# Kernel tuning notes

Hardware: AMD Instinct MI355X
Metric: run time of the kernel (lower is better)

Reference implementation:

```python
import jax, jax.numpy as jnp
import numpy as np

N_HEADS = 8

def setup_inputs() -> dict:
    key = jax.random.key(0)
    ks = jax.random.split(key, 8)
    N, D, H = 20000, 16, 256
    scale = np.float32(0.02)
    return {
        "h": jax.random.normal(ks[0], (N, H), dtype=jnp.float32),
        "attention_mask": jnp.zeros((N,), dtype=jnp.float32),
        "neighbor_idx": jax.random.randint(ks[1], (N, D), 0, N, dtype=jnp.int32),
        "Wq": jax.random.normal(ks[2], (H, H), dtype=jnp.float32) * scale,
        "bq": jnp.zeros((H,), dtype=jnp.float32),
        "Wk": jax.random.normal(ks[3], (H, H), dtype=jnp.float32) * scale,
        "bk": jnp.zeros((H,), dtype=jnp.float32),
        "Wv": jax.random.normal(ks[4], (H, H), dtype=jnp.float32) * scale,
        "bv": jnp.zeros((H,), dtype=jnp.float32),
    }

def reference(h, attention_mask, neighbor_idx, Wq, bq, Wk, bk, Wv, bv):
    N, H = h.shape
    nh = N_HEADS
    dh = H // nh
    inv_sqrt_dh = np.float32(1.0 / np.sqrt(dh))
    # query from each node's own state: [N, nh, dh]
    q = (h @ Wq.T + bq).reshape(N, nh, dh)
    # gather neighbor mailbox: [N, D, H]
    nb = h[neighbor_idx]
    k = (nb @ Wk.T + bk).reshape(N, -1, nh, dh)  # [N, D, nh, dh]
    v = (nb @ Wv.T + bv).reshape(N, -1, nh, dh)
    # scores: [N, nh, D]
    scores = jnp.einsum('nhd,nkhd->nhk', q, k) * inv_sqrt_dh
    # additive mask gathered from source nodes, broadcast over heads
    scores = scores + attention_mask[neighbor_idx][:, None, :]
    probs = jax.nn.softmax(scores, axis=-1)
    # dropout prob = 0.0 (eval) -> identity
    ctx = jnp.einsum('nhk,nkhd->nhd', probs, v).reshape(N, H)
    return ctx
```

## Files before the change

### kernel.cpp

```cpp
#include <hip/hip_runtime.h>
#include <hip/hip_fp16.h>
#include <math.h>

#define HDIM 256
#define DNEIGH 16

typedef __attribute__((ext_vector_type(8))) short short8;
typedef __attribute__((ext_vector_type(4))) float f32x4;

static __device__ __forceinline__ unsigned short f2bf(float f) {
    unsigned int u = __float_as_uint(f);
    unsigned int r = (u + 0x7fffu + ((u >> 16) & 1u)) >> 16;
    return (unsigned short)r;
}
static __device__ __forceinline__ float bf_lo(unsigned int u) {
    return __uint_as_float(u << 16);
}
static __device__ __forceinline__ float bf_hi(unsigned int u) {
    return __uint_as_float(u & 0xffff0000u);
}

#if __has_builtin(__builtin_amdgcn_cvt_pk_fp8_f32)
static __device__ __forceinline__ unsigned char f2fp8(float v) {
    int pk = __builtin_amdgcn_cvt_pk_fp8_f32(v, v, 0, false);
    return (unsigned char)(pk & 0xff);
}
#else
static __device__ __forceinline__ unsigned char f2fp8(float v) {
    unsigned short h = __half_as_ushort(__float2half(v * (1.0f / 256.0f)));
    unsigned short mag = h & 0x7fffu;
    mag = (unsigned short)((mag + 0x40u) >> 7);
    if (mag > 0x7f) mag = 0x7f;
    return (unsigned char)(((h >> 8) & 0x80u) | mag);
}
#endif

#if __has_builtin(__builtin_amdgcn_cvt_f32_fp8)
#define FP8D(u, i) __builtin_amdgcn_cvt_f32_fp8((u), (i))
#else
static __device__ __forceinline__ float fp8_byte_dec(unsigned int b) {
    unsigned int hb = ((b & 0x80u) << 8) | ((b & 0x7fu) << 7);
    return __half2float(__ushort_as_half((unsigned short)hb)) * 256.0f;
}
#define FP8D(u, i) fp8_byte_dec(((u) >> ((i) * 8)) & 0xffu)
#endif

static __device__ __forceinline__ void async_copy16(const void* g, void* l) {
    __builtin_amdgcn_global_load_lds(
        (const __attribute__((address_space(1))) unsigned int*)g,
        (__attribute__((address_space(3))) unsigned int*)l, 16, 0, 0);
}

__global__ __launch_bounds__(256) void cvt_kernel(
    const float* __restrict__ h,
    const float* __restrict__ wq, const float* __restrict__ wk, const float* __restrict__ wv,
    unsigned short* __restrict__ hb,
    unsigned short* __restrict__ wqb, unsigned short* __restrict__ wkb, unsigned short* __restrict__ wvb,
    int nh4)
{
    int i = blockIdx.x * 256 + threadIdx.x;
    const int total = nh4 + 3 * 16384;
    if (i >= total) return;
    const float4* src; unsigned short* dst; int off;
    if (i < nh4) { src = (const float4*)h; dst = hb; off = i; }
    else {
        int j = i - nh4; int s = j >> 14; off = j & 16383;
        src = (s == 0) ? (const float4*)wq : (s == 1) ? (const float4*)wk : (const float4*)wv;
        dst = (s == 0) ? wqb : (s == 1) ? wkb : wvb;
    }
    float4 v = src[off];
    ushort4 o;
    o.x = f2bf(v.x); o.y = f2bf(v.y); o.z = f2bf(v.z); o.w = f2bf(v.w);
    *(ushort4*)&dst[off * 4] = o;
}

__global__ __launch_bounds__(256) void qkv_mfma_kernel(
    const unsigned short* __restrict__ hb,
    const unsigned short* __restrict__ Wqb,
    const unsigned short* __restrict__ Wkb,
    const unsigned short* __restrict__ Wvb,
    const float* __restrict__ bq, const float* __restrict__ bk, const float* __restrict__ bv,
    unsigned short* __restrict__ Qb, unsigned char* __restrict__ K8,
    unsigned short* __restrict__ Vb,
    int N)
{
    __shared__ unsigned short As[128 * 64];
    __shared__ unsigned short Bs[128 * 64];

    const int t = threadIdx.x;
    const int lane = t & 63;
    const int wid = t >> 6;
    const int wm = wid >> 1;
    const int wn = wid & 1;
    const int m0 = blockIdx.x * 128;
    const int o0 = blockIdx.y * 128;
    const int sel = o0 >> 8;
    const int wrow0 = o0 & 255;

    const unsigned short* __restrict__ W = (sel == 0) ? Wqb : (sel == 1) ? Wkb : Wvb;
    const float* __restrict__ bias = (sel == 0) ? bq : (sel == 1) ? bk : bv;

    const int srow = lane >> 3;
    const int cg = (lane & 7) ^ srow;

    f32x4 acc[4][4] = {};

    for (int k0 = 0; k0 < HDIM; k0 += 64) {
#pragma unroll
        for (int r = 0; r < 4; ++r) {
            int rowb = wid * 32 + r * 8;
            const unsigned short* gp = &hb[(size_t)(m0 + rowb + srow) * HDIM + k0 + cg * 8];
            async_copy16(gp, &As[rowb * 64]);
        }
#pragma unroll
        for (int r = 0; r < 4; ++r) {
            int rowb = wid * 32 + r * 8;
            const unsigned short* gp = &W[(size_t)(wrow0 + rowb + srow) * HDIM + k0 + cg * 8];
            async_copy16(gp, &Bs[rowb * 64]);
        }
        __syncthreads();

#pragma unroll
        for (int ks = 0; ks < 2; ++ks) {
            short8 af[4], bf[4];
#pragma unroll
            for (int i = 0; i < 4; ++i) {
                int m = wm * 64 + i * 16 + (lane & 15);
                int chunk = (ks * 4 + (lane >> 4)) ^ (m & 7);
                af[i] = *(const short8*)&Bs[m * 64 + chunk * 8];
            }
#pragma unroll
            for (int j = 0; j < 4; ++j) {
                int n = wn * 64 + j * 16 + (lane & 15);
                int chunk = (ks * 4 + (lane >> 4)) ^ (n & 7);
                bf[j] = *(const short8*)&As[n * 64 + chunk * 8];
            }
#pragma unroll
            for (int i = 0; i < 4; ++i)
#pragma unroll
                for (int j = 0; j < 4; ++j)
                    acc[i][j] = __builtin_amdgcn_mfma_f32_16x16x32_bf16(af[i], bf[j], acc[i][j], 0, 0, 0);
        }
        __syncthreads();
    }

    const float qscale = 0.17677669529663688f;
#pragma unroll
    for (int i = 0; i < 4; ++i) {
        int ch = wrow0 + wm * 64 + i * 16 + (lane >> 4) * 4;
        float4 b4 = *(const float4*)&bias[ch];
#pragma unroll
        for (int j = 0; j < 4; ++j) {
            int node = m0 + wn * 64 + j * 16 + (lane & 15);
            if (node < N) {
                float v0 = acc[i][j][0] + b4.x;
                float v1 = acc[i][j][1] + b4.y;
                float v2 = acc[i][j][2] + b4.z;
                float v3 = acc[i][j][3] + b4.w;
                if (sel == 0) {
                    ushort4 o;
                    o.x = f2bf(v0 * qscale); o.y = f2bf(v1 * qscale);
                    o.z = f2bf(v2 * qscale); o.w = f2bf(v3 * qscale);
                    *(ushort4*)&Qb[(size_t)node * HDIM + ch] = o;
                } else if (sel == 1) {
                    uchar4 o;
                    o.x = f2fp8(v0); o.y = f2fp8(v1); o.z = f2fp8(v2); o.w = f2fp8(v3);
                    *(uchar4*)&K8[(size_t)node * HDIM + ch] = o;
                } else {
                    ushort4 o;
                    o.x = f2bf(v0); o.y = f2bf(v1); o.z = f2bf(v2); o.w = f2bf(v3);
                    *(ushort4*)&Vb[(size_t)node * HDIM + ch] = o;
                }
            }
        }
    }
}

__global__ __launch_bounds__(256) void attn4_kernel(
    const unsigned short* __restrict__ Qb,
    const unsigned char* __restrict__ K8,
    const unsigned short* __restrict__ Vb,
    const float* __restrict__ mask,
    const int* __restrict__ nidx,
    float* __restrict__ out,
    int N)
{
    const int w = threadIdx.x >> 6;
    const int lane = threadIdx.x & 63;
    const int n = blockIdx.x * 4 + w;
    if (n >= N) return;

    int idl = nidx[(size_t)n * DNEIGH + (lane & 15)];
    float mskl = mask[idl];

    unsigned int kreg[DNEIGH];
    uint2 vreg[DNEIGH];
#pragma unroll
    for (int d = 0; d < DNEIGH; ++d) {
        int id = __builtin_amdgcn_readlane(idl, d);
        kreg[d] = *(const unsigned int*)&K8[(size_t)id * HDIM + lane * 4];
        vreg[d] = *(const uint2*)&Vb[(size_t)id * HDIM + lane * 4];
    }

    uint2 qu = *(const uint2*)&Qb[(size_t)n * HDIM + lane * 4];
    const float q0 = bf_lo(qu.x), q1 = bf_hi(qu.x);
    const float q2 = bf_lo(qu.y), q3 = bf_hi(qu.y);

    float e[DNEIGH];
    float s = 0.f;
#pragma unroll
    for (int d = 0; d < DNEIGH; ++d) {
        float p = q0 * FP8D(kreg[d], 0) + q1 * FP8D(kreg[d], 1)
                + q2 * FP8D(kreg[d], 2) + q3 * FP8D(kreg[d], 3);
        p += __shfl_xor(p, 1);
        p += __shfl_xor(p, 2);
        p += __shfl_xor(p, 4);
        float mk = __int_as_float(__builtin_amdgcn_readlane(__float_as_int(mskl), d));
        e[d] = __expf(p + mk);
        s += e[d];
    }
    float rs = 1.f / s;

    float4 acc = make_float4(0.f, 0.f, 0.f, 0.f);
#pragma unroll
    for (int d = 0; d < DNEIGH; ++d) {
        float wgt = e[d] * rs;
        acc.x += wgt * bf_lo(vreg[d].x);
        acc.y += wgt * bf_hi(vreg[d].x);
        acc.z += wgt * bf_lo(vreg[d].y);
        acc.w += wgt * bf_hi(vreg[d].y);
    }
    *(float4*)&out[(size_t)n * HDIM + lane * 4] = acc;
}

extern "C" void kernel_launch(void* const* d_in, const int* in_sizes, int n_in,
                              void* d_out, int out_size, void* d_ws, size_t ws_size,
                              hipStream_t stream)
{
    const float* h    = (const float*)d_in[0];
    const float* mask = (const float*)d_in[1];
    const int*   nidx = (const int*)d_in[2];
    const float* Wq   = (const float*)d_in[3];
    const float* bq   = (const float*)d_in[4];
    const float* Wk   = (const float*)d_in[5];
    const float* bk   = (const float*)d_in[6];
    const float* Wv   = (const float*)d_in[7];
    const float* bv   = (const float*)d_in[8];

    const int N = in_sizes[0] / HDIM;

    char* ws = (char*)d_ws;
    unsigned short* Qbp = (unsigned short*)ws; ws += (size_t)N * HDIM * 2;
    unsigned short* Vbp = (unsigned short*)ws; ws += (size_t)N * HDIM * 2;
    unsigned short* hbp = (unsigned short*)ws; ws += (size_t)N * HDIM * 2;
    unsigned char*  K8p = (unsigned char*)ws;  ws += (size_t)N * HDIM;
    unsigned short* Wqb = (unsigned short*)ws; ws += 65536 * 2;
    unsigned short* Wkb = (unsigned short*)ws; ws += 65536 * 2;
    unsigned short* Wvb = (unsigned short*)ws;

    const int nh4 = (N * HDIM) / 4;
    const int total = nh4 + 3 * 16384;
    cvt_kernel<<<(total + 255) / 256, 256, 0, stream>>>(h, Wq, Wk, Wv, hbp, Wqb, Wkb, Wvb, nh4);

    dim3 g1((N + 127) / 128, 6);
    qkv_mfma_kernel<<<g1, 256, 0, stream>>>(hbp, Wqb, Wkb, Wvb, bq, bk, bv, Qbp, K8p, Vbp, N);

    attn4_kernel<<<(N + 3) / 4, 256, 0, stream>>>(Qbp, K8p, Vbp, mask, nidx, (float*)d_out, N);
}
```

Baseline: 142.8 us.

## Make QKV GEMM persistent with register-resident weights and double-buffered h tiles

The QKV projection kernel becomes persistent. It runs a fixed grid of 42x6 blocks, and each block loads its 128x256 weight slice into LDS once and keeps the A fragments in registers for all node tiles. It then loops over 64-node tiles and prefetches the next h tile into a second LDS buffer while computing the current one. This removes repeated weight loads and per-k-step barriers, at the cost of large register use (launch_bounds with min 1 block) and lower occupancy. Tail tiles rely on reading hb rows past N, as the original kernel also did.

```diff
diff --git a/kernel.cpp b/kernel.cpp
--- a/kernel.cpp
+++ b/kernel.cpp
@@ -74,7 +74,7 @@
     *(ushort4*)&dst[off * 4] = o;
 }
 
-__global__ __launch_bounds__(256) void qkv_mfma_kernel(
+__global__ __launch_bounds__(256, 1) void qkv_mfma_kernel(
     const unsigned short* __restrict__ hb,
     const unsigned short* __restrict__ Wqb,
     const unsigned short* __restrict__ Wkb,
@@ -84,15 +84,14 @@
     unsigned short* __restrict__ Vb,
     int N)
 {
-    __shared__ unsigned short As[128 * 64];
-    __shared__ unsigned short Bs[128 * 64];
+    __shared__ unsigned short Ws[128 * 256];
+    __shared__ unsigned short As[2][64 * 256];
 
     const int t = threadIdx.x;
     const int lane = t & 63;
     const int wid = t >> 6;
-    const int wm = wid >> 1;
-    const int wn = wid & 1;
-    const int m0 = blockIdx.x * 128;
+    const int wo = wid >> 1;
+    const int wn2 = wid & 1;
     const int o0 = blockIdx.y * 128;
     const int sel = o0 >> 8;
     const int wrow0 = o0 & 255;
@@ -100,79 +99,108 @@
     const unsigned short* __restrict__ W = (sel == 0) ? Wqb : (sel == 1) ? Wkb : Wvb;
     const float* __restrict__ bias = (sel == 0) ? bq : (sel == 1) ? bk : bv;
 
-    const int srow = lane >> 3;
-    const int cg = (lane & 7) ^ srow;
-
-    f32x4 acc[4][4] = {};
-
-    for (int k0 = 0; k0 < HDIM; k0 += 64) {
-#pragma unroll
-        for (int r = 0; r < 4; ++r) {
-            int rowb = wid * 32 + r * 8;
-            const unsigned short* gp = &hb[(size_t)(m0 + rowb + srow) * HDIM + k0 + cg * 8];
-            async_copy16(gp, &As[rowb * 64]);
-        }
-#pragma unroll
-        for (int r = 0; r < 4; ++r) {
-            int rowb = wid * 32 + r * 8;
-            const unsigned short* gp = &W[(size_t)(wrow0 + rowb + srow) * HDIM + k0 + cg * 8];
-            async_copy16(gp, &Bs[rowb * 64]);
-        }
-        __syncthreads();
-
-#pragma unroll
-        for (int ks = 0; ks < 2; ++ks) {
-            short8 af[4], bf[4];
-#pragma unroll
-            for (int i = 0; i < 4; ++i) {
-                int m = wm * 64 + i * 16 + (lane & 15);
-                int chunk = (ks * 4 + (lane >> 4)) ^ (m & 7);
-                af[i] = *(const short8*)&Bs[m * 64 + chunk * 8];
+    const int ntiles = (N + 63) >> 6;
+    const int BX = gridDim.x;
+
+    const int p = lane & 31;
+    const int rhalf = lane >> 5;
+
+#pragma unroll
+    for (int r = 0; r < 16; ++r) {
+        int lr = wid * 32 + r * 2 + rhalf;
+        int c = (p & ~7) | ((p ^ lr) & 7);
+        const unsigned short* gp = &W[(size_t)(wrow0 + lr) * 256 + c * 8];
+        async_copy16(gp, &Ws[(wid * 32 + r * 2) * 256]);
+    }
+    {
+        int g0 = blockIdx.x * 64;
+#pragma unroll
+        for (int r = 0; r < 8; ++r) {
+            int lr = wid * 16 + r * 2 + rhalf;
+            int c = (p & ~7) | ((p ^ lr) & 7);
+            const unsigned short* gp = &hb[(size_t)(g0 + lr) * 256 + c * 8];
+            async_copy16(gp, &As[0][(wid * 16 + r * 2) * 256]);
+        }
+    }
+    __syncthreads();
+
+    short8 af[8][4];
+#pragma unroll
+    for (int ks = 0; ks < 8; ++ks)
+#pragma unroll
+        for (int i = 0; i < 4; ++i) {
+            int m = wo * 64 + i * 16 + (lane & 15);
+            int c = ks * 4 + (lane >> 4);
+            int pos = (c & ~7) | ((c ^ m) & 7);
+            af[ks][i] = *(const short8*)&Ws[m * 256 + pos * 8];
+        }
+
+    const float qscale = 0.17677669529663688f;
+
+    int tile = blockIdx.x;
+    for (int it = 0; tile < ntiles; ++it, tile += BX) {
+        int cur = it & 1;
+        int nxt = tile + BX;
+        if (nxt < ntiles) {
+            int g0 = nxt * 64;
+#pragma unroll
+            for (int r = 0; r < 8; ++r) {
+                int lr = wid * 16 + r * 2 + rhalf;
+                int c = (p & ~7) | ((p ^ lr) & 7);
+                const unsigned short* gp = &hb[(size_t)(g0 + lr) * 256 + c * 8];
+                async_copy16(gp, &As[cur ^ 1][(wid * 16 + r * 2) * 256]);
             }
-#pragma unroll
-            for (int j = 0; j < 4; ++j) {
-                int n = wn * 64 + j * 16 + (lane & 15);
-                int chunk = (ks * 4 + (lane >> 4)) ^ (n & 7);
-                bf[j] = *(const short8*)&As[n * 64 + chunk * 8];
+        }
+
+        f32x4 acc[4][2] = {};
+#pragma unroll
+        for (int ks = 0; ks < 8; ++ks) {
+            short8 bf[2];
+#pragma unroll
+            for (int j = 0; j < 2; ++j) {
+                int n = wn2 * 32 + j * 16 + (lane & 15);
+                int c = ks * 4 + (lane >> 4);
+                int pos = (c & ~7) | ((c ^ n) & 7);
+                bf[j] = *(const short8*)&As[cur][n * 256 + pos * 8];
             }
 #pragma unroll
             for (int i = 0; i < 4; ++i)
 #pragma unroll
-                for (int j = 0; j < 4; ++j)
-                    acc[i][j] = __builtin_amdgcn_mfma_f32_16x16x32_bf16(af[i], bf[j], acc[i][j], 0, 0, 0);
-        }
-        __syncthreads();
-    }
-
-    const float qscale = 0.17677669529663688f;
-#pragma unroll
-    for (int i = 0; i < 4; ++i) {
-        int ch = wrow0 + wm * 64 + i * 16 + (lane >> 4) * 4;
-        float4 b4 = *(const float4*)&bias[ch];
-#pragma unroll
-        for (int j = 0; j < 4; ++j) {
-            int node = m0 + wn * 64 + j * 16 + (lane & 15);
-            if (node < N) {
-                float v0 = acc[i][j][0] + b4.x;
-                float v1 = acc[i][j][1] + b4.y;
-                float v2 = acc[i][j][2] + b4.z;
-                float v3 = acc[i][j][3] + b4.w;
-                if (sel == 0) {
-                    ushort4 o;
-                    o.x = f2bf(v0 * qscale); o.y = f2bf(v1 * qscale);
-                    o.z = f2bf(v2 * qscale); o.w = f2bf(v3 * qscale);
-                    *(ushort4*)&Qb[(size_t)node * HDIM + ch] = o;
-                } else if (sel == 1) {
-                    uchar4 o;
-                    o.x = f2fp8(v0); o.y = f2fp8(v1); o.z = f2fp8(v2); o.w = f2fp8(v3);
-                    *(uchar4*)&K8[(size_t)node * HDIM + ch] = o;
-                } else {
-                    ushort4 o;
-                    o.x = f2bf(v0); o.y = f2bf(v1); o.z = f2bf(v2); o.w = f2bf(v3);
-                    *(ushort4*)&Vb[(size_t)node * HDIM + ch] = o;
+                for (int j = 0; j < 2; ++j)
+                    acc[i][j] = __builtin_amdgcn_mfma_f32_16x16x32_bf16(af[ks][i], bf[j], acc[i][j], 0, 0, 0);
+        }
+
+        int nodeb = tile * 64;
+#pragma unroll
+        for (int i = 0; i < 4; ++i) {
+            int ch = wrow0 + wo * 64 + i * 16 + (lane >> 4) * 4;
+            float4 b4 = *(const float4*)&bias[ch];
+#pragma unroll
+            for (int j = 0; j < 2; ++j) {
+                int node = nodeb + wn2 * 32 + j * 16 + (lane & 15);
+                if (node < N) {
+                    float v0 = acc[i][j][0] + b4.x;
+                    float v1 = acc[i][j][1] + b4.y;
+                    float v2 = acc[i][j][2] + b4.z;
+                    float v3 = acc[i][j][3] + b4.w;
+                    if (sel == 0) {
+                        ushort4 o;
+                        o.x = f2bf(v0 * qscale); o.y = f2bf(v1 * qscale);
+                        o.z = f2bf(v2 * qscale); o.w = f2bf(v3 * qscale);
+                        *(ushort4*)&Qb[(size_t)node * HDIM + ch] = o;
+                    } else if (sel == 1) {
+                        uchar4 o;
+                        o.x = f2fp8(v0); o.y = f2fp8(v1); o.z = f2fp8(v2); o.w = f2fp8(v3);
+                        *(uchar4*)&K8[(size_t)node * HDIM + ch] = o;
+                    } else {
+                        ushort4 o;
+                        o.x = f2bf(v0); o.y = f2bf(v1); o.z = f2bf(v2); o.w = f2bf(v3);
+                        *(ushort4*)&Vb[(size_t)node * HDIM + ch] = o;
+                    }
                 }
             }
         }
+        __syncthreads();
     }
 }
 
@@ -210,13 +238,13 @@
     float s = 0.f;
 #pragma unroll
     for (int d = 0; d < DNEIGH; ++d) {
-        float p = q0 * FP8D(kreg[d], 0) + q1 * FP8D(kreg[d], 1)
-                + q2 * FP8D(kreg[d], 2) + q3 * FP8D(kreg[d], 3);
-        p += __shfl_xor(p, 1);
-        p += __shfl_xor(p, 2);
-        p += __shfl_xor(p, 4);
+        float pdot = q0 * FP8D(kreg[d], 0) + q1 * FP8D(kreg[d], 1)
+                   + q2 * FP8D(kreg[d], 2) + q3 * FP8D(kreg[d], 3);
+        pdot += __shfl_xor(pdot, 1);
+        pdot += __shfl_xor(pdot, 2);
+        pdot += __shfl_xor(pdot, 4);
         float mk = __int_as_float(__builtin_amdgcn_readlane(__float_as_int(mskl), d));
-        e[d] = __expf(p + mk);
+        e[d] = __expf(pdot + mk);
         s += e[d];
     }
     float rs = 1.f / s;
@@ -262,7 +290,7 @@
     const int total = nh4 + 3 * 16384;
     cvt_kernel<<<(total + 255) / 256, 256, 0, stream>>>(h, Wq, Wk, Wv, hbp, Wqb, Wkb, Wvb, nh4);
 
-    dim3 g1((N + 127) / 128, 6);
+    dim3 g1(42, 6);
     qkv_mfma_kernel<<<g1, 256, 0, stream>>>(hbp, Wqb, Wkb, Wvb, bq, bk, bv, Qbp, K8p, Vbp, N);
 
     attn4_kernel<<<(N + 3) / 4, 256, 0, stream>>>(Qbp, K8p, Vbp, mask, nidx, (float*)d_out, N);
```

Result: faster. 137.5 us, median of 2 (-3.7%).
